# Kernel optimization log

Hardware: AMD Instinct MI355X
Metric: run time of the kernel (lower is better)

Reference implementation:

```python
import jax, jax.numpy as jnp
import numpy as np

N_NEURON = 1024
N_PEPTIDE = 16
N_GENES = 1
BATCH = 2048
SQ = 32  # int(sqrt(N_NEURON))
DT = 1.0 / 120.0
STATE_SIZE = N_NEURON + N_GENES + N_NEURON + N_NEURON * N_PEPTIDE  # 18433


def setup_inputs() -> dict:
    key = jax.random.key(0)
    ks = jax.random.split(key, 10)
    # structured state: [ablate_mat | pc2 | neuron | peptide]
    ablate_mat = jnp.ones((BATCH, N_NEURON), jnp.float32)
    pc2 = jax.random.uniform(ks[0], (BATCH, N_GENES), jnp.float32)
    neuron = jax.random.normal(ks[1], (BATCH, N_NEURON), jnp.float32)
    peptide = jax.random.uniform(ks[2], (BATCH, N_NEURON * N_PEPTIDE), jnp.float32)
    state = jnp.concatenate([ablate_mat, pc2, neuron, peptide], axis=-1)
    u = jax.random.normal(ks[3], (BATCH, 1), jnp.float32)
    # uniform noise sample used by the exp firing noise; keep strictly < 1
    noise_u = jax.random.uniform(ks[4], (BATCH, N_NEURON), jnp.float32, 1e-6, 1.0 - 1e-6)
    D = jax.random.uniform(ks[5], (N_PEPTIDE,), jnp.float32)
    pep_prod_rate = jax.random.uniform(ks[6], (N_PEPTIDE,), jnp.float32)
    pep_decay_rate = jax.random.uniform(ks[7], (N_PEPTIDE,), jnp.float32)
    pep_action = jax.random.normal(ks[8], (N_PEPTIDE,), jnp.float32)
    synapse_matrix = jax.random.normal(ks[9], (N_NEURON, N_NEURON), jnp.float32) * 0.02
    neuron_decay = jnp.ones((1,), jnp.float32) * 0.5
    input_layer = jax.random.normal(jax.random.fold_in(key, 11), (N_NEURON,), jnp.float32)
    return dict(u=u, state=state, noise_u=noise_u, D=D, pep_prod_rate=pep_prod_rate,
                pep_decay_rate=pep_decay_rate, pep_action=pep_action,
                synapse_matrix=synapse_matrix, neuron_decay=neuron_decay,
                input_layer=input_layer)


def reference(u, state, noise_u, D, pep_prod_rate, pep_decay_rate, pep_action,
              synapse_matrix, neuron_decay, input_layer):
    # func = abs (log_train=False)
    Dp = jnp.abs(D)
    prod_r = jnp.abs(pep_prod_rate)
    decay_r = jnp.abs(pep_decay_rate)
    ndecay = jnp.abs(neuron_decay)

    # unpack state: [ablate | pc2 | neuron | peptide]
    ablate_mat = state[:, :N_NEURON]
    pc2 = state[:, N_NEURON:N_NEURON + N_GENES]
    neuron = state[:, N_NEURON + N_GENES:2 * N_NEURON + N_GENES]
    pep_flat = state[:, 2 * N_NEURON + N_GENES:]
    peptide = pep_flat.reshape(-1, N_NEURON, N_PEPTIDE)

    firing = jax.nn.relu(neuron) * ablate_mat
    neuron = neuron * ablate_mat

    # noisy_fire, noise='exp': firing = -(firing+0.01)*log(1-U)
    firing = -(firing + 0.01) * jnp.log1p(-noise_u)
    firing = jnp.clip(firing, 0.0, 10.0)

    # peptide production / decay
    pep_prod = prod_r * firing[:, :, None]           # (b, n, p)
    pep_decay = decay_r * peptide                    # (b, n, p)

    # wrap-around 2D Laplacian diffusion stencil on (SQ, SQ) grid
    ps = peptide.reshape(-1, SQ, SQ, N_PEPTIDE)
    lap = (jnp.roll(ps, -1, axis=1) + jnp.roll(ps, 1, axis=1)
           + jnp.roll(ps, -1, axis=2) + jnp.roll(ps, 1, axis=2) - 4.0 * ps)
    pep_diffuse = (Dp * lap).reshape(-1, N_NEURON, N_PEPTIDE)

    # neuron dynamics
    d_neuron = jnp.sum(peptide * pep_action, axis=-1) * pc2
    d_neuron = d_neuron + firing @ synapse_matrix
    d_neuron = d_neuron - neuron * ndecay
    d_neuron = d_neuron + input_layer * u            # (b,1)*(n,) broadcast

    d_peptide = (pep_prod - pep_decay + pep_diffuse).reshape(-1, N_NEURON * N_PEPTIDE)
    pep_new = pep_flat + d_peptide * DT
    neuron_new = (neuron + d_neuron * DT) * ablate_mat

    state_new = jnp.concatenate([ablate_mat, pc2, neuron_new, pep_new], axis=-1)
    # return_firing=True
    return firing, state_new
```

## Files before the change

### kernel.cpp

```cpp
#include <hip/hip_runtime.h>
#include <hip/hip_bf16.h>

#define N_NEURON 1024
#define N_PEPTIDE 16
#define N_GENES 1
#define BATCH 2048
#define SQ 32
#define DT_STEP (1.0f/120.0f)
#define S_STRIDE (N_NEURON + N_GENES + N_NEURON + N_NEURON*N_PEPTIDE)

typedef __attribute__((ext_vector_type(8))) short short8;
typedef __attribute__((ext_vector_type(4))) float floatx4;
typedef __attribute__((ext_vector_type(2))) float floatx2;
typedef floatx4 floatx4u __attribute__((aligned(4)));
typedef floatx2 floatx2u __attribute__((aligned(4)));

__global__ __launch_bounds__(256) void synT_cast(const float* __restrict__ syn,
                                                 __hip_bfloat16* __restrict__ synT) {
    __shared__ float tile[32][33];
    const int n0 = blockIdx.x * 32;
    const int k0 = blockIdx.y * 32;
    const int tx = threadIdx.x & 31;
    const int ty = threadIdx.x >> 5;
    #pragma unroll
    for (int i = 0; i < 4; ++i)
        tile[ty + i*8][tx] = syn[(long)(k0 + ty + i*8) * N_NEURON + n0 + tx];
    __syncthreads();
    #pragma unroll
    for (int i = 0; i < 4; ++i)
        synT[(long)(n0 + ty + i*8) * N_NEURON + k0 + tx] =
            __float2bfloat16(tile[tx][ty + i*8]);
}

__global__ __launch_bounds__(512) void pep_fused(
    const float* __restrict__ u,
    const float* __restrict__ state,
    const float* __restrict__ noise,
    const float* __restrict__ D,
    const float* __restrict__ prod_g,
    const float* __restrict__ decay_g,
    const float* __restrict__ pact_g,
    const float* __restrict__ ndecay_g,
    const float* __restrict__ inL,
    float* __restrict__ firing_out,
    float* __restrict__ state_new,
    __hip_bfloat16* __restrict__ fbf)
{
    __shared__ floatx4 slab4[4096];
    __shared__ float sf[N_NEURON];
    __shared__ float sn[N_NEURON];
    __shared__ float sps[N_NEURON];

    const int b   = blockIdx.x;
    const int tid = threadIdx.x;
    const long bS = (long)b * S_STRIDE;
    const float u_b  = u[b];
    const float pc2  = state[bS + N_NEURON];
    const float ndecay = fabsf(ndecay_g[0]);

    const float* __restrict__ pep = state + bS + 2 * N_NEURON + N_GENES;
    float* __restrict__ pep_new = state_new + bS + 2 * N_NEURON + N_GENES;

    const int pq = tid & 3;
    const int nl = tid >> 2;
    const int p0q = pq * 4;
    floatx4 Dq, prq, deq, paq;
    #pragma unroll
    for (int j = 0; j < 4; ++j) {
        Dq[j]  = fabsf(D[p0q + j]);
        prq[j] = fabsf(prod_g[p0q + j]);
        deq[j] = fabsf(decay_g[p0q + j]);
        paq[j] = pact_g[p0q + j];
    }

    floatx4 sl[8];
    #pragma unroll
    for (int k = 0; k < 8; ++k)
        sl[k] = *(const floatx4u*)(pep + (tid + k * 512) * 4);

    const int gn = tid * 2;
    floatx2 abv = *(const floatx2u*)(state + bS + gn);
    floatx2 nrv = *(const floatx2u*)(state + bS + N_NEURON + N_GENES + gn);
    floatx2 nzv = *(const floatx2*)(noise + (long)b * N_NEURON + gn);

    #pragma unroll
    for (int k = 0; k < 8; ++k)
        slab4[tid + k * 512] = sl[k];

    #pragma unroll
    for (int k = 0; k < 8; ++k) {
        const int n = k * 128 + nl;
        float ps = sl[k][0]*paq[0] + sl[k][1]*paq[1] + sl[k][2]*paq[2] + sl[k][3]*paq[3];
        ps += __shfl_xor(ps, 1);
        ps += __shfl_xor(ps, 2);
        if (pq == 0) sps[n] = ps;
    }

    {
        floatx2 fv, nmv;
        #pragma unroll
        for (int j = 0; j < 2; ++j) {
            nmv[j] = nrv[j] * abv[j];
            float fr = fmaxf(nrv[j], 0.f) * abv[j];
            fr = -(fr + 0.01f) * log1pf(-nzv[j]);
            fr = fminf(fmaxf(fr, 0.f), 10.f);
            fv[j] = fr;
        }
        __builtin_nontemporal_store(fv, (floatx2*)(firing_out + (long)b * N_NEURON + gn));
        __hip_bfloat16 h0 = __float2bfloat16(fv[0]);
        __hip_bfloat16 h1 = __float2bfloat16(fv[1]);
        unsigned int packed = (unsigned int)(*(unsigned short*)&h0) |
                              ((unsigned int)(*(unsigned short*)&h1) << 16);
        *(unsigned int*)(fbf + (long)b * N_NEURON + gn) = packed;
        __builtin_nontemporal_store(abv, (floatx2u*)(state_new + bS + gn));
        *(floatx2*)(sf + gn) = fv;
        *(floatx2*)(sn + gn) = nmv;
    }
    if (tid == 0) state_new[bS + N_NEURON] = pc2;
    __syncthreads();

    #pragma unroll
    for (int it = 0; it < 8; ++it) {
        const int n  = it * 128 + nl;
        const int si = n >> 5, sj = n & 31;
        const floatx4 c  = sl[it];
        const floatx4 vu = slab4[((((si + 31) & 31) * 32) + sj) * 4 + pq];
        const floatx4 vd = slab4[((((si +  1) & 31) * 32) + sj) * 4 + pq];
        const floatx4 vl = slab4[((si * 32) + ((sj + 31) & 31)) * 4 + pq];
        const floatx4 vr = slab4[((si * 32) + ((sj +  1) & 31)) * 4 + pq];
        const float fn = sf[n];
        floatx4 lap = vu + vd + vl + vr - 4.f * c;
        floatx4 outv = c + DT_STEP * (prq * fn - deq * c + Dq * lap);
        __builtin_nontemporal_store(outv, (floatx4u*)(pep_new + (n << 4) + p0q));
    }
    __syncthreads();

    {
        floatx2 ss = *(const floatx2*)(sps + gn);
        floatx2 nm = *(const floatx2*)(sn + gn);
        floatx2 il = *(const floatx2*)(inL + gn);
        floatx2 c0;
        #pragma unroll
        for (int j = 0; j < 2; ++j)
            c0[j] = nm[j] + DT_STEP * (ss[j] * pc2 - nm[j] * ndecay + il[j] * u_b);
        *(floatx2u*)(state_new + bS + N_NEURON + N_GENES + gn) = c0;
    }
}

__device__ __forceinline__ void stage8k(const __hip_bfloat16* __restrict__ gbase,
                                        char* lhalf, int row0, int k0,
                                        int w, int lane)
{
    #pragma unroll
    for (int i = 0; i < 2; ++i) {
        const int ch  = w * 2 + i;
        const int o   = ch * 1024 + lane * 16;
        const int row = o >> 7;
        const int c16 = (o >> 4) & 7;
        const int cl  = c16 ^ (row & 7);
        const __hip_bfloat16* g = gbase + (long)(row0 + row) * 1024 + k0 + cl * 8;
        __builtin_amdgcn_global_load_lds(
            (const __attribute__((address_space(1))) void*)g,
            (__attribute__((address_space(3))) void*)(lhalf + ch * 1024),
            16, 0, 0);
    }
}

__device__ __forceinline__ short8 lds_frag(const char* lhalf, int row, int c16) {
    const int cl = c16 ^ (row & 7);
    return *(const short8*)(lhalf + row * 128 + cl * 16);
}

__global__ __launch_bounds__(256) void gemm_epi(
    const __hip_bfloat16* __restrict__ A,
    const __hip_bfloat16* __restrict__ BT,
    const float* __restrict__ state,
    float* __restrict__ state_new)
{
    __shared__ __align__(16) char lds[2][16384];
    const int tid = threadIdx.x;
    const int w = tid >> 6, lane = tid & 63;
    const int q = lane >> 4, l16 = lane & 15;
    const int m0 = blockIdx.x * 64;
    const int n0 = blockIdx.y * 64;
    const int wm = (w & 1) * 32, wn = (w >> 1) * 32;

    float abv[2][2][4], c0v[2][2][4];
    #pragma unroll
    for (int mi = 0; mi < 2; ++mi)
    #pragma unroll
    for (int ni = 0; ni < 2; ++ni)
    #pragma unroll
    for (int r = 0; r < 4; ++r) {
        const int m = m0 + wm + mi * 16 + q * 4 + r;
        const int n = n0 + wn + ni * 16 + l16;
        const long sidx = (long)m * S_STRIDE;
        abv[mi][ni][r] = state[sidx + n];
        c0v[mi][ni][r] = state_new[sidx + N_NEURON + N_GENES + n];
    }

    floatx4 acc[2][2] = {};

    stage8k(A,  lds[0],        m0, 0, w, lane);
    stage8k(BT, lds[0] + 8192, n0, 0, w, lane);
    __syncthreads();

#define GEMM_STEP(CUR, T)                                                     \
    {                                                                         \
        if ((T) < 15) {                                                       \
            stage8k(A,  lds[(CUR) ^ 1],        m0, ((T) + 1) * 64, w, lane);  \
            stage8k(BT, lds[(CUR) ^ 1] + 8192, n0, ((T) + 1) * 64, w, lane);  \
        }                                                                     \
        const char* la = lds[(CUR)];                                          \
        const char* lb = lds[(CUR)] + 8192;                                   \
        _Pragma("unroll")                                                     \
        for (int kk = 0; kk < 2; ++kk) {                                      \
            const int c16 = kk * 4 + q;                                       \
            short8 a0 = lds_frag(la, wm + l16,      c16);                     \
            short8 a1 = lds_frag(la, wm + 16 + l16, c16);                     \
            short8 b0 = lds_frag(lb, wn + l16,      c16);                     \
            short8 b1 = lds_frag(lb, wn + 16 + l16, c16);                     \
            acc[0][0] = __builtin_amdgcn_mfma_f32_16x16x32_bf16(a0, b0, acc[0][0], 0, 0, 0); \
            acc[0][1] = __builtin_amdgcn_mfma_f32_16x16x32_bf16(a0, b1, acc[0][1], 0, 0, 0); \
            acc[1][0] = __builtin_amdgcn_mfma_f32_16x16x32_bf16(a1, b0, acc[1][0], 0, 0, 0); \
            acc[1][1] = __builtin_amdgcn_mfma_f32_16x16x32_bf16(a1, b1, acc[1][1], 0, 0, 0); \
        }                                                                     \
        if ((T) < 15) __syncthreads();                                        \
    }

    #pragma unroll
    for (int tt = 0; tt < 8; ++tt) {
        GEMM_STEP(0, tt * 2)
        GEMM_STEP(1, tt * 2 + 1)
    }
#undef GEMM_STEP

    #pragma unroll
    for (int mi = 0; mi < 2; ++mi)
    #pragma unroll
    for (int ni = 0; ni < 2; ++ni)
    #pragma unroll
    for (int r = 0; r < 4; ++r) {
        const int m = m0 + wm + mi * 16 + q * 4 + r;
        const int n = n0 + wn + ni * 16 + l16;
        const long sidx = (long)m * S_STRIDE;
        state_new[sidx + N_NEURON + N_GENES + n] =
            (c0v[mi][ni][r] + DT_STEP * acc[mi][ni][r]) * abv[mi][ni][r];
    }
}

extern "C" void kernel_launch(void* const* d_in, const int* in_sizes, int n_in,
                              void* d_out, int out_size, void* d_ws, size_t ws_size,
                              hipStream_t stream) {
    const float* u      = (const float*)d_in[0];
    const float* state  = (const float*)d_in[1];
    const float* noise  = (const float*)d_in[2];
    const float* D      = (const float*)d_in[3];
    const float* prod   = (const float*)d_in[4];
    const float* decay  = (const float*)d_in[5];
    const float* pact   = (const float*)d_in[6];
    const float* syn    = (const float*)d_in[7];
    const float* ndec   = (const float*)d_in[8];
    const float* inL    = (const float*)d_in[9];

    float* firing = (float*)d_out;
    float* state_new = firing + (long)BATCH * N_NEURON;

    __hip_bfloat16* fbf  = (__hip_bfloat16*)d_ws;
    __hip_bfloat16* synT = fbf + (long)BATCH * N_NEURON;

    hipLaunchKernelGGL(synT_cast, dim3(32, 32), dim3(256), 0, stream, syn, synT);
    hipLaunchKernelGGL(pep_fused, dim3(BATCH), dim3(512), 0, stream,
                       u, state, noise, D, prod, decay, pact, ndec, inL,
                       firing, state_new, fbf);
    hipLaunchKernelGGL(gemm_epi, dim3(32, 16), dim3(256), 0, stream,
                       fbf, synT, state, state_new);
}
```

Before: 316.1 us.

## Split fused peptide kernel into firing kernel and fine-grained stencil stream kernel

Replaces the single per-batch peptide kernel, which staged the whole 64KB slab in LDS, with two kernels. The first computes firing and its bf16 copy. The second runs 16 small blocks per batch row that read the stencil neighbours straight from global memory and compute the peptide and neuron updates. This removes the large LDS footprint and the barriers, aiming for higher occupancy and more memory parallelism. In exchange it adds a launch, a firing round-trip through global memory, and redundant neighbour reads that rely on cache hits.

```diff
diff --git a/kernel.cpp b/kernel.cpp
--- a/kernel.cpp
+++ b/kernel.cpp
@@ -10,6 +10,7 @@
 #define S_STRIDE (N_NEURON + N_GENES + N_NEURON + N_NEURON*N_PEPTIDE)
 
 typedef __attribute__((ext_vector_type(8))) short short8;
+typedef __attribute__((ext_vector_type(4))) short short4v;
 typedef __attribute__((ext_vector_type(4))) float floatx4;
 typedef __attribute__((ext_vector_type(2))) float floatx2;
 typedef floatx4 floatx4u __attribute__((aligned(4)));
@@ -32,38 +33,72 @@
             __float2bfloat16(tile[tx][ty + i*8]);
 }
 
-__global__ __launch_bounds__(512) void pep_fused(
+__global__ __launch_bounds__(256) void firing_k(
+    const float* __restrict__ state,
+    const float* __restrict__ noise,
+    float* __restrict__ firing_out,
+    float* __restrict__ state_new,
+    __hip_bfloat16* __restrict__ fbf)
+{
+    const int b = blockIdx.x;
+    const int tid = threadIdx.x;
+    const long bS = (long)b * S_STRIDE;
+    const int n4 = tid * 4;
+
+    floatx4 ab = *(const floatx4u*)(state + bS + n4);
+    floatx4 nr = *(const floatx4u*)(state + bS + N_NEURON + N_GENES + n4);
+    floatx4 nz = *(const floatx4*)(noise + (long)b * N_NEURON + n4);
+    floatx4 f;
+    short4v hb;
+    #pragma unroll
+    for (int j = 0; j < 4; ++j) {
+        float fr = fmaxf(nr[j], 0.f) * ab[j];
+        fr = -(fr + 0.01f) * log1pf(-nz[j]);
+        fr = fminf(fmaxf(fr, 0.f), 10.f);
+        f[j] = fr;
+        __hip_bfloat16 h = __float2bfloat16(fr);
+        hb[j] = *reinterpret_cast<short*>(&h);
+    }
+    *(floatx4*)(firing_out + (long)b * N_NEURON + n4) = f;
+    *(short4v*)(fbf + (long)b * N_NEURON + n4) = hb;
+    __builtin_nontemporal_store(ab, (floatx4u*)(state_new + bS + n4));
+    if (tid == 0) state_new[bS + N_NEURON] = state[bS + N_NEURON];
+}
+
+__global__ __launch_bounds__(256) void pep_stream(
     const float* __restrict__ u,
     const float* __restrict__ state,
-    const float* __restrict__ noise,
     const float* __restrict__ D,
     const float* __restrict__ prod_g,
     const float* __restrict__ decay_g,
     const float* __restrict__ pact_g,
     const float* __restrict__ ndecay_g,
     const float* __restrict__ inL,
-    float* __restrict__ firing_out,
-    float* __restrict__ state_new,
-    __hip_bfloat16* __restrict__ fbf)
-{
-    __shared__ floatx4 slab4[4096];
-    __shared__ float sf[N_NEURON];
-    __shared__ float sn[N_NEURON];
-    __shared__ float sps[N_NEURON];
-
-    const int b   = blockIdx.x;
+    const float* __restrict__ firing,
+    float* __restrict__ state_new)
+{
+    const int g   = blockIdx.x;
+    const int b   = g >> 4;
+    const int n0  = (g & 15) * 64;
     const int tid = threadIdx.x;
+    const int pq  = tid & 3;
+    const int nl  = tid >> 2;
+    const int p0q = pq * 4;
+    const int n   = n0 + nl;
+    const int si  = n >> 5, sj = n & 31;
     const long bS = (long)b * S_STRIDE;
-    const float u_b  = u[b];
-    const float pc2  = state[bS + N_NEURON];
-    const float ndecay = fabsf(ndecay_g[0]);
 
     const float* __restrict__ pep = state + bS + 2 * N_NEURON + N_GENES;
     float* __restrict__ pep_new = state_new + bS + 2 * N_NEURON + N_GENES;
 
-    const int pq = tid & 3;
-    const int nl = tid >> 2;
-    const int p0q = pq * 4;
+    const int idx = (n << 4) + p0q;
+    const floatx4 c  = *(const floatx4u*)(pep + idx);
+    const floatx4 vu = *(const floatx4u*)(pep + ((((si + 31) & 31) * 32 + sj) << 4) + p0q);
+    const floatx4 vd = *(const floatx4u*)(pep + ((((si +  1) & 31) * 32 + sj) << 4) + p0q);
+    const floatx4 vl = *(const floatx4u*)(pep + ((si * 32 + ((sj + 31) & 31)) << 4) + p0q);
+    const floatx4 vr = *(const floatx4u*)(pep + ((si * 32 + ((sj +  1) & 31)) << 4) + p0q);
+    const float fn = firing[(long)b * N_NEURON + n];
+
     floatx4 Dq, prq, deq, paq;
     #pragma unroll
     for (int j = 0; j < 4; ++j) {
@@ -73,77 +108,22 @@
         paq[j] = pact_g[p0q + j];
     }
 
-    floatx4 sl[8];
-    #pragma unroll
-    for (int k = 0; k < 8; ++k)
-        sl[k] = *(const floatx4u*)(pep + (tid + k * 512) * 4);
-
-    const int gn = tid * 2;
-    floatx2 abv = *(const floatx2u*)(state + bS + gn);
-    floatx2 nrv = *(const floatx2u*)(state + bS + N_NEURON + N_GENES + gn);
-    floatx2 nzv = *(const floatx2*)(noise + (long)b * N_NEURON + gn);
-
-    #pragma unroll
-    for (int k = 0; k < 8; ++k)
-        slab4[tid + k * 512] = sl[k];
-
-    #pragma unroll
-    for (int k = 0; k < 8; ++k) {
-        const int n = k * 128 + nl;
-        float ps = sl[k][0]*paq[0] + sl[k][1]*paq[1] + sl[k][2]*paq[2] + sl[k][3]*paq[3];
-        ps += __shfl_xor(ps, 1);
-        ps += __shfl_xor(ps, 2);
-        if (pq == 0) sps[n] = ps;
-    }
-
-    {
-        floatx2 fv, nmv;
-        #pragma unroll
-        for (int j = 0; j < 2; ++j) {
-            nmv[j] = nrv[j] * abv[j];
-            float fr = fmaxf(nrv[j], 0.f) * abv[j];
-            fr = -(fr + 0.01f) * log1pf(-nzv[j]);
-            fr = fminf(fmaxf(fr, 0.f), 10.f);
-            fv[j] = fr;
-        }
-        __builtin_nontemporal_store(fv, (floatx2*)(firing_out + (long)b * N_NEURON + gn));
-        __hip_bfloat16 h0 = __float2bfloat16(fv[0]);
-        __hip_bfloat16 h1 = __float2bfloat16(fv[1]);
-        unsigned int packed = (unsigned int)(*(unsigned short*)&h0) |
-                              ((unsigned int)(*(unsigned short*)&h1) << 16);
-        *(unsigned int*)(fbf + (long)b * N_NEURON + gn) = packed;
-        __builtin_nontemporal_store(abv, (floatx2u*)(state_new + bS + gn));
-        *(floatx2*)(sf + gn) = fv;
-        *(floatx2*)(sn + gn) = nmv;
-    }
-    if (tid == 0) state_new[bS + N_NEURON] = pc2;
-    __syncthreads();
-
-    #pragma unroll
-    for (int it = 0; it < 8; ++it) {
-        const int n  = it * 128 + nl;
-        const int si = n >> 5, sj = n & 31;
-        const floatx4 c  = sl[it];
-        const floatx4 vu = slab4[((((si + 31) & 31) * 32) + sj) * 4 + pq];
-        const floatx4 vd = slab4[((((si +  1) & 31) * 32) + sj) * 4 + pq];
-        const floatx4 vl = slab4[((si * 32) + ((sj + 31) & 31)) * 4 + pq];
-        const floatx4 vr = slab4[((si * 32) + ((sj +  1) & 31)) * 4 + pq];
-        const float fn = sf[n];
-        floatx4 lap = vu + vd + vl + vr - 4.f * c;
-        floatx4 outv = c + DT_STEP * (prq * fn - deq * c + Dq * lap);
-        __builtin_nontemporal_store(outv, (floatx4u*)(pep_new + (n << 4) + p0q));
-    }
-    __syncthreads();
-
-    {
-        floatx2 ss = *(const floatx2*)(sps + gn);
-        floatx2 nm = *(const floatx2*)(sn + gn);
-        floatx2 il = *(const floatx2*)(inL + gn);
-        floatx2 c0;
-        #pragma unroll
-        for (int j = 0; j < 2; ++j)
-            c0[j] = nm[j] + DT_STEP * (ss[j] * pc2 - nm[j] * ndecay + il[j] * u_b);
-        *(floatx2u*)(state_new + bS + N_NEURON + N_GENES + gn) = c0;
+    floatx4 lap = vu + vd + vl + vr - 4.f * c;
+    floatx4 outv = c + DT_STEP * (prq * fn - deq * c + Dq * lap);
+    __builtin_nontemporal_store(outv, (floatx4u*)(pep_new + idx));
+
+    float ps = c[0]*paq[0] + c[1]*paq[1] + c[2]*paq[2] + c[3]*paq[3];
+    ps += __shfl_xor(ps, 1);
+    ps += __shfl_xor(ps, 2);
+    if (pq == 0) {
+        const float ab_ = state[bS + n];
+        const float nr_ = state[bS + N_NEURON + N_GENES + n];
+        const float nm  = nr_ * ab_;
+        const float pc2 = state[bS + N_NEURON];
+        const float ndecay = fabsf(ndecay_g[0]);
+        const float u_b = u[b];
+        const float c0 = nm + DT_STEP * (ps * pc2 - nm * ndecay + inL[n] * u_b);
+        state_new[bS + N_NEURON + N_GENES + n] = c0;
     }
 }
 
@@ -270,9 +250,11 @@
     __hip_bfloat16* synT = fbf + (long)BATCH * N_NEURON;
 
     hipLaunchKernelGGL(synT_cast, dim3(32, 32), dim3(256), 0, stream, syn, synT);
-    hipLaunchKernelGGL(pep_fused, dim3(BATCH), dim3(512), 0, stream,
-                       u, state, noise, D, prod, decay, pact, ndec, inL,
-                       firing, state_new, fbf);
+    hipLaunchKernelGGL(firing_k, dim3(BATCH), dim3(256), 0, stream,
+                       state, noise, firing, state_new, fbf);
+    hipLaunchKernelGGL(pep_stream, dim3(BATCH * 16), dim3(256), 0, stream,
+                       u, state, D, prod, decay, pact, ndec, inL,
+                       firing, state_new);
     hipLaunchKernelGGL(gemm_epi, dim3(32, 16), dim3(256), 0, stream,
                        fbf, synT, state, state_new);
 }
```

Result: no change. 318.1 us (+0.6%).
